# Kernel optimization log

Hardware: AMD Instinct MI355X
Metric: run time of the kernel (lower is better)

## Reference

```python
import jax, jax.numpy as jnp
import numpy as np

N_NODES = 100000
N_EDGES = 1600000
D = 128


def _gine_layer(x, src, dst, e, W1, b1, W2, b2):
    # message: relu(x_j + e_ji), aggregate: sum at destination
    m = jax.nn.relu(x[src] + e)                       # [E, D]
    agg = jax.ops.segment_sum(m, dst, num_segments=x.shape[0])  # [N, D]
    h = agg + x                                       # (1 + eps) * x_i with eps = 0
    h = jax.nn.relu(jnp.dot(h, W1) + b1)
    return jnp.dot(h, W2) + b2


def setup_inputs() -> dict:
    key = jax.random.key(0)
    ks = jax.random.split(key, 16)
    s = 0.05
    inp = {
        "x": jax.random.normal(ks[0], (N_NODES, D), dtype=jnp.float32),
        "edge_index": jax.random.randint(ks[1], (2, N_EDGES), 0, N_NODES, dtype=jnp.int64) if jax.config.jax_enable_x64 else jax.random.randint(ks[1], (2, N_EDGES), 0, N_NODES, dtype=jnp.int32),
        "edge_attr": jax.random.randint(ks[2], (N_EDGES,), 0, 100, dtype=jnp.int32),
        "edge_emb": jax.random.normal(ks[3], (100, D), dtype=jnp.float32) * s,
        "Win": jax.random.normal(ks[4], (D, D), dtype=jnp.float32) * s,
        "b_in": jnp.zeros((D,), dtype=jnp.float32),
        "W1_0": jax.random.normal(ks[5], (D, D), dtype=jnp.float32) * s,
        "b1_0": jnp.zeros((D,), dtype=jnp.float32),
        "W2_0": jax.random.normal(ks[6], (D, D), dtype=jnp.float32) * s,
        "b2_0": jnp.zeros((D,), dtype=jnp.float32),
        "W1_1": jax.random.normal(ks[7], (D, D), dtype=jnp.float32) * s,
        "b1_1": jnp.zeros((D,), dtype=jnp.float32),
        "W2_1": jax.random.normal(ks[8], (D, D), dtype=jnp.float32) * s,
        "b2_1": jnp.zeros((D,), dtype=jnp.float32),
        "Wout": jax.random.normal(ks[9], (D, 1), dtype=jnp.float32) * s,
        "b_out": jnp.zeros((1,), dtype=jnp.float32),
    }
    return inp


def reference(x, edge_index, edge_attr, edge_emb, Win, b_in,
              W1_0, b1_0, W2_0, b2_0, W1_1, b1_1, W2_1, b2_1,
              Wout, b_out):
    src, dst = edge_index[0], edge_index[1]
    e = edge_emb[edge_attr]                 # [E, D] edge-attribute embedding lookup
    h = jnp.dot(x, Win) + b_in              # input_proj
    # layer 0: GINEConv + residual add + relu (norm=none, dropout off)
    h = jax.nn.relu(_gine_layer(h, src, dst, e, W1_0, b1_0, W2_0, b2_0) + h)
    # layer 1
    h = jax.nn.relu(_gine_layer(h, src, dst, e, W1_1, b1_1, W2_1, b2_1) + h)
    # output_mlp: single Linear(hidden, 1); no final activation, no pooling
    return jnp.dot(h, Wout) + b_out
```

## Files before the change

kernel.cpp:

```cpp
#include <hip/hip_runtime.h>

#define NN 100000
#define D 128
#define CHUNK 4096
#define BCSTRIDE 392
#define AGG_BLOCKS 1024

typedef __attribute__((ext_vector_type(8))) short short8;
typedef __attribute__((ext_vector_type(8))) unsigned short ushort8;
typedef __attribute__((ext_vector_type(4))) float f32x4;

__device__ __forceinline__ float4 ld4(const float* p) { return *(const float4*)p; }

__device__ __forceinline__ unsigned short f2bf(float f) {
    unsigned int u = __float_as_uint(f);
    unsigned int r = u + 0x7fffu + ((u >> 16) & 1u);
    return (unsigned short)(r >> 16);
}
__device__ __forceinline__ float bf2f(unsigned short h) {
    return __uint_as_float(((unsigned int)h) << 16);
}
__device__ __forceinline__ int swz(int r, int c) {
    return r * 128 + ((((c >> 2) ^ (r & 7)) << 2) | (c & 3));
}

__device__ __forceinline__ void coop_gemm8(
    const unsigned int* uT,
    const unsigned short* __restrict__ Whi, const unsigned short* __restrict__ Wlo,
    int wv, int lane, int lr, int q, f32x4 acc[4])
{
    #pragma unroll
    for (int ks = 0; ks < 4; ++ks) {
        short8 ahi[4], alo[4];
        #pragma unroll
        for (int m = 0; m < 4; ++m) {
            const int row = m * 16 + lr;
            const int cb  = ks * 32 + q * 8;
            const uint4 a0 = *(const uint4*)&uT[swz(row, cb)];
            const uint4 a1 = *(const uint4*)&uT[swz(row, cb + 4)];
            const unsigned int w[8] = {a0.x, a0.y, a0.z, a0.w, a1.x, a1.y, a1.z, a1.w};
            #pragma unroll
            for (int j = 0; j < 8; ++j) {
                ahi[m][j] = (short)(w[j] >> 16);
                alo[m][j] = (short)(w[j] & 0xffffu);
            }
        }
        const int base = ((wv * 4 + ks) * 64 + lane) * 8;
        const short8 bhi = *(const short8*)&Whi[base];
        const short8 blo = *(const short8*)&Wlo[base];
        #pragma unroll
        for (int m = 0; m < 4; ++m) {
            acc[m] = __builtin_amdgcn_mfma_f32_16x16x32_bf16(alo[m], bhi, acc[m], 0, 0, 0);
            acc[m] = __builtin_amdgcn_mfma_f32_16x16x32_bf16(ahi[m], blo, acc[m], 0, 0, 0);
            acc[m] = __builtin_amdgcn_mfma_f32_16x16x32_bf16(ahi[m], bhi, acc[m], 0, 0, 0);
        }
    }
}

__device__ __forceinline__ void gemm_in_body(
    unsigned int* uT, int bid,
    const float* __restrict__ A1,
    const unsigned short* __restrict__ Whi, const unsigned short* __restrict__ Wlo,
    const float* __restrict__ bias,
    unsigned short* __restrict__ out_hi, unsigned short* __restrict__ out_lo, int N)
{
    const int t    = threadIdx.x;
    const int wv   = t >> 6;
    const int lane = t & 63;
    const int lr   = lane & 15;
    const int q    = lane >> 4;
    const int rE   = wv * 8 + (lane >> 3);
    const int cE   = (lane & 7) * 16;
    const int rowE = bid * 64 + rE;

    {
        float v[16];
        if (rowE < N) {
            const int off = rowE * D + cE;
            #pragma unroll
            for (int k = 0; k < 4; ++k) {
                const float4 x = ld4(&A1[off + k * 4]);
                v[k * 4 + 0] = x.x; v[k * 4 + 1] = x.y; v[k * 4 + 2] = x.z; v[k * 4 + 3] = x.w;
            }
        } else {
            #pragma unroll
            for (int j = 0; j < 16; ++j) v[j] = 0.f;
        }
        #pragma unroll
        for (int k = 0; k < 4; ++k) {
            unsigned int pk[4];
            #pragma unroll
            for (int j = 0; j < 4; ++j) {
                const float f = v[k * 4 + j];
                const unsigned int hi = f2bf(f);
                pk[j] = (hi << 16) | f2bf(f - bf2f((unsigned short)hi));
            }
            *(uint4*)&uT[swz(rE, cE + k * 4)] = make_uint4(pk[0], pk[1], pk[2], pk[3]);
        }
    }
    __syncthreads();

    f32x4 acc[4];
    #pragma unroll
    for (int m = 0; m < 4; ++m) acc[m] = (f32x4){0.f, 0.f, 0.f, 0.f};
    coop_gemm8(uT, Whi, Wlo, wv, lane, lr, q, acc);
    __syncthreads();

    {
        const float b = bias[wv * 16 + lr];
        #pragma unroll
        for (int m = 0; m < 4; ++m)
            #pragma unroll
            for (int r = 0; r < 4; ++r)
                uT[swz(m * 16 + q * 4 + r, wv * 16 + lr)] = __float_as_uint(acc[m][r] + b);
    }
    __syncthreads();

    if (rowE < N) {
        const int off = rowE * D + cE;
        unsigned int w[16];
        #pragma unroll
        for (int k = 0; k < 4; ++k) {
            const uint4 a = *(const uint4*)&uT[swz(rE, cE + k * 4)];
            w[k * 4 + 0] = a.x; w[k * 4 + 1] = a.y; w[k * 4 + 2] = a.z; w[k * 4 + 3] = a.w;
        }
        #pragma unroll
        for (int h8 = 0; h8 < 2; ++h8) {
            ushort8 oh, ol;
            #pragma unroll
            for (int j = 0; j < 8; ++j) {
                const float o = __uint_as_float(w[h8 * 8 + j]);
                const unsigned short h = f2bf(o);
                oh[j] = h;
                ol[j] = f2bf(o - bf2f(h));
            }
            *(ushort8*)&out_hi[off + h8 * 8] = oh;
            *(ushort8*)&out_lo[off + h8 * 8] = ol;
        }
    }
}

__global__ __launch_bounds__(256) void setup_all(
    const float* __restrict__ W0, const float* __restrict__ W1,
    const float* __restrict__ W2, const float* __restrict__ W3,
    const float* __restrict__ W4, unsigned short* __restrict__ wp,
    const float* __restrict__ emb, unsigned int* __restrict__ embp,
    int* __restrict__ binTotal)
{
    const int T = blockIdx.x * 256 + threadIdx.x;
    if (T < 5 * D * D) {
        const int w = T / (D * D);
        const int t = T % (D * D);
        const float* W = (w == 0) ? W0 : (w == 1) ? W1 : (w == 2) ? W2 : (w == 3) ? W3 : W4;
        const int j  = t & 7;
        const int L  = (t >> 3) & 63;
        const int ks = (t >> 9) & 3;
        const int nt = t >> 11;
        const float v = W[(ks * 32 + (L >> 4) * 8 + j) * D + nt * 16 + (L & 15)];
        const unsigned short h = f2bf(v);
        unsigned short* hi = wp + (size_t)w * 2 * D * D;
        hi[t] = h;
        hi[D * D + t] = f2bf(v - bf2f(h));
    } else if (T < 5 * D * D + 6400) {
        const int i = T - 5 * D * D;
        embp[i] = (unsigned int)f2bf(emb[i * 2]) | ((unsigned int)f2bf(emb[i * 2 + 1]) << 16);
    } else if (T < 5 * D * D + 6400 + BCSTRIDE) {
        binTotal[T - 5 * D * D - 6400] = 0;
    }
}

__global__ __launch_bounds__(512, 8) void fuse_count_gemm(
    const int* __restrict__ dst, int* __restrict__ blkcnt,
    int* __restrict__ binTotal, int E, int nbins, int csrB,
    const float* __restrict__ A1,
    const unsigned short* __restrict__ Whi, const unsigned short* __restrict__ Wlo,
    const float* __restrict__ bias,
    unsigned short* __restrict__ out_hi, unsigned short* __restrict__ out_lo,
    int N, int gemmBase)
{
    __shared__ __align__(16) unsigned int uT[64 * 128];
    if ((int)blockIdx.x < csrB) {
        int* hist = (int*)uT;
        const int t = threadIdx.x;
        const int i = blockIdx.x;
        for (int k = t; k < nbins; k += 512) hist[k] = 0;
        __syncthreads();
        const int e0 = i * CHUNK;
        const int e1 = min(E, e0 + CHUNK);
        for (int e = e0 + t; e < e1; e += 512) atomicAdd(&hist[dst[e] >> 8], 1);
        __syncthreads();
        for (int k = t; k < nbins; k += 512) {
            const int c = hist[k];
            blkcnt[i * BCSTRIDE + k] = c;
            if (c) atomicAdd(&binTotal[k], c);
        }
    } else {
        gemm_in_body(uT, blockIdx.x - csrB + gemmBase, A1, Whi, Wlo, bias, out_hi, out_lo, N);
    }
}

__global__ __launch_bounds__(512) void bin_scan(
    const int* __restrict__ binTotal, int* __restrict__ binStart,
    int* __restrict__ binCursor, int nbins)
{
    __shared__ int s[512];
    const int t = threadIdx.x;
    const int v = (t < nbins) ? binTotal[t] : 0;
    s[t] = v;
    __syncthreads();
    for (int off = 1; off < 512; off <<= 1) {
        const int x = (t >= off) ? s[t - off] : 0;
        __syncthreads();
        s[t] += x;
        __syncthreads();
    }
    if (t < nbins) { binStart[t] = s[t] - v; binCursor[t] = s[t] - v; }
    if (t == 0)    binStart[nbins] = s[511];
}

__global__ __launch_bounds__(512, 8) void fuse_scatter_gemm(
    const int* __restrict__ src, const int* __restrict__ dst,
    const int* __restrict__ attr, const int* __restrict__ blkcnt,
    int* __restrict__ binCursor, int2* __restrict__ binned, int E, int nbins, int csrB,
    const float* __restrict__ A1,
    const unsigned short* __restrict__ Whi, const unsigned short* __restrict__ Wlo,
    const float* __restrict__ bias,
    unsigned short* __restrict__ out_hi, unsigned short* __restrict__ out_lo,
    int N, int gemmBase)
{
    __shared__ __align__(16) unsigned int uT[64 * 128];
    if ((int)blockIdx.x < csrB) {
        int* cur = (int*)uT;
        const int t = threadIdx.x;
        const int i = blockIdx.x;
        for (int k = t; k < nbins; k += 512) {
            const int c = blkcnt[i * BCSTRIDE + k];
            if (c) cur[k] = atomicAdd(&binCursor[k], c);
        }
        __syncthreads();
        const int e0 = i * CHUNK;
        const int e1 = min(E, e0 + CHUNK);
        for (int e = e0 + t; e < e1; e += 512) {
            const int d = dst[e];
            const int p = atomicAdd(&cur[d >> 8], 1);
            binned[p] = make_int2(src[e] | (attr[e] << 20), d);
        }
    } else {
        gemm_in_body(uT, blockIdx.x - csrB + gemmBase, A1, Whi, Wlo, bias, out_hi, out_lo, N);
    }
}

__global__ __launch_bounds__(512, 8) void fuse_build_gemm(
    const int2* __restrict__ binned, const int* __restrict__ binStart,
    int* __restrict__ rowptr, int* __restrict__ epack, int csrB,
    const float* __restrict__ A1,
    const unsigned short* __restrict__ Whi, const unsigned short* __restrict__ Wlo,
    const float* __restrict__ bias,
    unsigned short* __restrict__ out_hi, unsigned short* __restrict__ out_lo,
    int N, int gemmBase)
{
    __shared__ __align__(16) unsigned int uT[64 * 128];
    if ((int)blockIdx.x < csrB) {
        int* hist = (int*)uT;
        int* scn  = (int*)uT + 256;
        int* curn = (int*)uT + 512;
        const int t = threadIdx.x;
        const int b = blockIdx.x;
        if (t < 256) hist[t] = 0;
        __syncthreads();
        const int ebeg = binStart[b];
        const int eend = binStart[b + 1];
        for (int e = ebeg + t; e < eend; e += 512) atomicAdd(&hist[binned[e].y & 255], 1);
        __syncthreads();
        if (t < 256) scn[t] = hist[t];
        __syncthreads();
        for (int off = 1; off < 256; off <<= 1) {
            int x = 0;
            if (t < 256 && t >= off) x = scn[t - off];
            __syncthreads();
            if (t < 256) scn[t] += x;
            __syncthreads();
        }
        if (t < 256) {
            const int node = b * 256 + t;
            if (node < N) rowptr[node] = ebeg + scn[t];
            curn[t] = ebeg + scn[t] - hist[t];
        }
        __syncthreads();
        for (int e = ebeg + t; e < eend; e += 512) {
            const int2 v = binned[e];
            const int p = atomicAdd(&curn[v.y & 255], 1);
            epack[p] = v.x;
        }
    } else {
        gemm_in_body(uT, blockIdx.x - csrB + gemmBase, A1, Whi, Wlo, bias, out_hi, out_lo, N);
    }
}

template<bool LAST>
__global__ __launch_bounds__(512, 8) void mlp_fused(
    const float* __restrict__ agg,
    const unsigned short* h_hi, const unsigned short* h_lo,
    const unsigned short* __restrict__ W1hi, const unsigned short* __restrict__ W1lo,
    const float* __restrict__ b1,
    const unsigned short* __restrict__ W2hi, const unsigned short* __restrict__ W2lo,
    const float* __restrict__ b2,
    unsigned short* out_hi, unsigned short* out_lo,
    const float* __restrict__ Wout, const float* __restrict__ bout,
    float* __restrict__ outv, int N)
{
    __shared__ __align__(16) unsigned int uT[64 * 128];
    const int t    = threadIdx.x;
    const int wv   = t >> 6;
    const int lane = t & 63;
    const int lr   = lane & 15;
    const int q    = lane >> 4;
    const int rE   = wv * 8 + (lane >> 3);
    const int cE   = (lane & 7) * 16;
    const int rowE = blockIdx.x * 64 + rE;

    {
        float v[16];
        if (rowE < N) {
            const int off = rowE * D + cE;
            #pragma unroll
            for (int k = 0; k < 4; ++k) {
                const float4 x = ld4(&agg[off + k * 4]);
                v[k * 4 + 0] = x.x; v[k * 4 + 1] = x.y; v[k * 4 + 2] = x.z; v[k * 4 + 3] = x.w;
            }
            #pragma unroll
            for (int h8 = 0; h8 < 2; ++h8) {
                const ushort8 hh = *(const ushort8*)&h_hi[off + h8 * 8];
                const ushort8 ll = *(const ushort8*)&h_lo[off + h8 * 8];
                #pragma unroll
                for (int j = 0; j < 8; ++j) v[h8 * 8 + j] += bf2f(hh[j]) + bf2f(ll[j]);
            }
        } else {
            #pragma unroll
            for (int j = 0; j < 16; ++j) v[j] = 0.f;
        }
        #pragma unroll
        for (int k = 0; k < 4; ++k) {
            unsigned int pk[4];
            #pragma unroll
            for (int j = 0; j < 4; ++j) {
                const float f = v[k * 4 + j];
                const unsigned int hi = f2bf(f);
                pk[j] = (hi << 16) | f2bf(f - bf2f((unsigned short)hi));
            }
            *(uint4*)&uT[swz(rE, cE + k * 4)] = make_uint4(pk[0], pk[1], pk[2], pk[3]);
        }
    }
    __syncthreads();

    f32x4 acc[4];
    #pragma unroll
    for (int m = 0; m < 4; ++m) acc[m] = (f32x4){0.f, 0.f, 0.f, 0.f};
    coop_gemm8(uT, W1hi, W1lo, wv, lane, lr, q, acc);
    __syncthreads();

    {
        const float b = b1[wv * 16 + lr];
        #pragma unroll
        for (int m = 0; m < 4; ++m)
            #pragma unroll
            for (int r = 0; r < 4; ++r) {
                const float o = fmaxf(acc[m][r] + b, 0.f);
                const unsigned int hi = f2bf(o);
                const unsigned int lo = f2bf(o - bf2f((unsigned short)hi));
                uT[swz(m * 16 + q * 4 + r, wv * 16 + lr)] = (hi << 16) | lo;
            }
    }
    __syncthreads();

    f32x4 acc2[4];
    #pragma unroll
    for (int m = 0; m < 4; ++m) acc2[m] = (f32x4){0.f, 0.f, 0.f, 0.f};
    coop_gemm8(uT, W2hi, W2lo, wv, lane, lr, q, acc2);
    __syncthreads();

    {
        const float b = b2[wv * 16 + lr];
        #pragma unroll
        for (int m = 0; m < 4; ++m)
            #pragma unroll
            for (int r = 0; r < 4; ++r)
                uT[swz(m * 16 + q * 4 + r, wv * 16 + lr)] = __float_as_uint(acc2[m][r] + b);
    }
    __syncthreads();

    if (LAST) {
        float accv = 0.f;
        if (rowE < N) {
            const int off = rowE * D + cE;
            unsigned int w[16];
            #pragma unroll
            for (int k = 0; k < 4; ++k) {
                const uint4 a = *(const uint4*)&uT[swz(rE, cE + k * 4)];
                w[k * 4 + 0] = a.x; w[k * 4 + 1] = a.y; w[k * 4 + 2] = a.z; w[k * 4 + 3] = a.w;
            }
            #pragma unroll
            for (int h8 = 0; h8 < 2; ++h8) {
                const ushort8 hh = *(const ushort8*)&h_hi[off + h8 * 8];
                const ushort8 ll = *(const ushort8*)&h_lo[off + h8 * 8];
                const float4 w0 = ld4(&Wout[cE + h8 * 8]);
                const float4 w1 = ld4(&Wout[cE + h8 * 8 + 4]);
                float o[8];
                #pragma unroll
                for (int j = 0; j < 8; ++j)
                    o[j] = fmaxf(__uint_as_float(w[h8 * 8 + j]) + bf2f(hh[j]) + bf2f(ll[j]), 0.f);
                accv += o[0] * w0.x + o[1] * w0.y + o[2] * w0.z + o[3] * w0.w;
                accv += o[4] * w1.x + o[5] * w1.y + o[6] * w1.z + o[7] * w1.w;
            }
        }
        accv += __shfl_xor(accv, 1);
        accv += __shfl_xor(accv, 2);
        accv += __shfl_xor(accv, 4);
        if ((lane & 7) == 0 && rowE < N) outv[rowE] = accv + bout[0];
    } else if (rowE < N) {
        const int off = rowE * D + cE;
        unsigned int w[16];
        #pragma unroll
        for (int k = 0; k < 4; ++k) {
            const uint4 a = *(const uint4*)&uT[swz(rE, cE + k * 4)];
            w[k * 4 + 0] = a.x; w[k * 4 + 1] = a.y; w[k * 4 + 2] = a.z; w[k * 4 + 3] = a.w;
        }
        #pragma unroll
        for (int h8 = 0; h8 < 2; ++h8) {
            const ushort8 hh = *(const ushort8*)&h_hi[off + h8 * 8];
            const ushort8 ll = *(const ushort8*)&h_lo[off + h8 * 8];
            ushort8 oh, ol;
            #pragma unroll
            for (int j = 0; j < 8; ++j) {
                const float o = fmaxf(__uint_as_float(w[h8 * 8 + j]) + bf2f(hh[j]) + bf2f(ll[j]), 0.f);
                const unsigned short h = f2bf(o);
                oh[j] = h;
                ol[j] = f2bf(o - bf2f(h));
            }
            *(ushort8*)&out_hi[off + h8 * 8] = oh;
            *(ushort8*)&out_lo[off + h8 * 8] = ol;
        }
    }
}

__global__ __launch_bounds__(512) void aggregate(
    const unsigned int* __restrict__ hu,
    const int* __restrict__ rowptr, const int* __restrict__ epack,
    const unsigned int* __restrict__ embp, float* __restrict__ agg, int N)
{
    __shared__ unsigned int semb[100 * 64];
    const int t = threadIdx.x;
    for (int i = t; i < 100 * 64; i += 512) semb[i] = embp[i];
    __syncthreads();

    const int wv   = t >> 6;
    const int lane = t & 63;

    for (int node = blockIdx.x * 8 + wv; node < N; node += AGG_BLOCKS * 8) {
        int start = (node == 0) ? 0 : rowptr[node - 1];
        int end   = rowptr[node];
        start = __builtin_amdgcn_readfirstlane(start);
        end   = __builtin_amdgcn_readfirstlane(end);

        float ax = 0.f, ay = 0.f;
        int j = start;

        for (; j < end && (j & 3); ++j) {
            const int p0 = __builtin_amdgcn_readfirstlane(epack[j]);
            const unsigned int u0 = hu[(p0 & 0xFFFFF) * 64 + lane];
            const unsigned int v0 = semb[(p0 >> 20) * 64 + lane];
            ax += fmaxf(__uint_as_float(u0 << 16) + __uint_as_float(v0 << 16), 0.f);
            ay += fmaxf(__uint_as_float(u0 & 0xffff0000u) + __uint_as_float(v0 & 0xffff0000u), 0.f);
        }

        for (; j + 7 < end; j += 8) {
            const int4 pk0 = *(const int4*)&epack[j];
            const int4 pk1 = *(const int4*)&epack[j + 4];
            int p[8];
            p[0] = __builtin_amdgcn_readfirstlane(pk0.x);
            p[1] = __builtin_amdgcn_readfirstlane(pk0.y);
            p[2] = __builtin_amdgcn_readfirstlane(pk0.z);
            p[3] = __builtin_amdgcn_readfirstlane(pk0.w);
            p[4] = __builtin_amdgcn_readfirstlane(pk1.x);
            p[5] = __builtin_amdgcn_readfirstlane(pk1.y);
            p[6] = __builtin_amdgcn_readfirstlane(pk1.z);
            p[7] = __builtin_amdgcn_readfirstlane(pk1.w);
            unsigned int u[8], v[8];
            #pragma unroll
            for (int k = 0; k < 8; ++k) u[k] = hu[(p[k] & 0xFFFFF) * 64 + lane];
            #pragma unroll
            for (int k = 0; k < 8; ++k) v[k] = semb[(p[k] >> 20) * 64 + lane];
            #pragma unroll
            for (int k = 0; k < 8; ++k) {
                ax += fmaxf(__uint_as_float(u[k] << 16) + __uint_as_float(v[k] << 16), 0.f);
                ay += fmaxf(__uint_as_float(u[k] & 0xffff0000u) + __uint_as_float(v[k] & 0xffff0000u), 0.f);
            }
        }

        if (j + 3 < end) {
            const int4 pk0 = *(const int4*)&epack[j];
            int p[4];
            p[0] = __builtin_amdgcn_readfirstlane(pk0.x);
            p[1] = __builtin_amdgcn_readfirstlane(pk0.y);
            p[2] = __builtin_amdgcn_readfirstlane(pk0.z);
            p[3] = __builtin_amdgcn_readfirstlane(pk0.w);
            unsigned int u[4], v[4];
            #pragma unroll
            for (int k = 0; k < 4; ++k) u[k] = hu[(p[k] & 0xFFFFF) * 64 + lane];
            #pragma unroll
            for (int k = 0; k < 4; ++k) v[k] = semb[(p[k] >> 20) * 64 + lane];
            #pragma unroll
            for (int k = 0; k < 4; ++k) {
                ax += fmaxf(__uint_as_float(u[k] << 16) + __uint_as_float(v[k] << 16), 0.f);
                ay += fmaxf(__uint_as_float(u[k] & 0xffff0000u) + __uint_as_float(v[k] & 0xffff0000u), 0.f);
            }
            j += 4;
        }

        for (; j < end; ++j) {
            const int p0 = __builtin_amdgcn_readfirstlane(epack[j]);
            const unsigned int u0 = hu[(p0 & 0xFFFFF) * 64 + lane];
            const unsigned int v0 = semb[(p0 >> 20) * 64 + lane];
            ax += fmaxf(__uint_as_float(u0 << 16) + __uint_as_float(v0 << 16), 0.f);
            ay += fmaxf(__uint_as_float(u0 & 0xffff0000u) + __uint_as_float(v0 & 0xffff0000u), 0.f);
        }

        float2 o; o.x = ax; o.y = ay;
        ((float2*)agg)[node * 64 + lane] = o;
    }
}

extern "C" void kernel_launch(void* const* d_in, const int* in_sizes, int n_in,
                              void* d_out, int out_size, void* d_ws, size_t ws_size,
                              hipStream_t stream)
{
    const float* x     = (const float*)d_in[0];
    const int*   ei    = (const int*)  d_in[1];
    const int*   attr  = (const int*)  d_in[2];
    const float* emb   = (const float*)d_in[3];
    const float* Win   = (const float*)d_in[4];
    const float* b_in  = (const float*)d_in[5];
    const float* W1_0  = (const float*)d_in[6];
    const float* b1_0  = (const float*)d_in[7];
    const float* W2_0  = (const float*)d_in[8];
    const float* b2_0  = (const float*)d_in[9];
    const float* W1_1  = (const float*)d_in[10];
    const float* b1_1  = (const float*)d_in[11];
    const float* W2_1  = (const float*)d_in[12];
    const float* b2_1  = (const float*)d_in[13];
    const float* Wout  = (const float*)d_in[14];
    const float* b_out = (const float*)d_in[15];
    float* out = (float*)d_out;

    const int N = NN;
    const int E = in_sizes[2];
    const int* srcp = ei;
    const int* dstp = ei + E;
    const int nbins = (N + 255) >> 8;
    const int eblocks = (E + CHUNK - 1) / CHUNK;

    unsigned short* h_hi = (unsigned short*)d_ws;
    unsigned short* h_lo = h_hi + (size_t)N * D;
    float* agg    = (float*)(h_lo + (size_t)N * D);
    int*   rowptr = (int*)(agg + (size_t)N * D);
    int*   epack  = rowptr + N;
    unsigned short* wp = (unsigned short*)(epack + E);
    unsigned short* Whi[5], *Wlo[5];
    for (int i = 0; i < 5; ++i) {
        Whi[i] = wp + (size_t)i * 2 * D * D;
        Wlo[i] = Whi[i] + D * D;
    }
    unsigned int* embp = (unsigned int*)(wp + 5 * 2 * D * D);
    int2* binned    = (int2*)agg;
    int*  blkcnt    = (int*)(binned + E);
    int*  binTotal  = blkcnt + eblocks * BCSTRIDE;
    int*  binStart  = binTotal + BCSTRIDE;
    int*  binCursor = binStart + BCSTRIDE;

    const int fgrid = (N + 63) / 64;
    const int sgrid = (5 * D * D + 6400 + BCSTRIDE + 255) / 256;

    const int G1 = 200;
    const int G2 = 700;
    const int G3 = fgrid - G1 - G2;

    setup_all<<<sgrid, dim3(256), 0, stream>>>(Win, W1_0, W2_0, W1_1, W2_1, wp, emb, embp, binTotal);

    fuse_count_gemm<<<eblocks + G1, dim3(512), 0, stream>>>(
        dstp, blkcnt, binTotal, E, nbins, eblocks,
        x, Whi[0], Wlo[0], b_in, h_hi, h_lo, N, 0);
    bin_scan<<<1, 512, 0, stream>>>(binTotal, binStart, binCursor, nbins);
    fuse_scatter_gemm<<<eblocks + G2, dim3(512), 0, stream>>>(
        srcp, dstp, attr, blkcnt, binCursor, binned, E, nbins, eblocks,
        x, Whi[0], Wlo[0], b_in, h_hi, h_lo, N, G1);
    fuse_build_gemm<<<nbins + G3, dim3(512), 0, stream>>>(
        binned, binStart, rowptr, epack, nbins,
        x, Whi[0], Wlo[0], b_in, h_hi, h_lo, N, G1 + G2);

    aggregate<<<AGG_BLOCKS, dim3(512), 0, stream>>>(
        (const unsigned int*)h_hi, rowptr, epack, embp, agg, N);
    mlp_fused<false><<<fgrid, dim3(512), 0, stream>>>(
        agg, h_hi, h_lo, Whi[1], Wlo[1], b1_0, Whi[2], Wlo[2], b2_0,
        h_hi, h_lo, nullptr, nullptr, nullptr, N);

    aggregate<<<AGG_BLOCKS, dim3(512), 0, stream>>>(
        (const unsigned int*)h_hi, rowptr, epack, embp, agg, N);
    mlp_fused<true><<<fgrid, dim3(512), 0, stream>>>(
        agg, h_hi, h_lo, Whi[3], Wlo[3], b1_1, Whi[4], Wlo[4], b2_1,
        nullptr, nullptr, Wout, b_out, out, N);
}
```

Measured before the change: 418.9 us.

## Split wavefront into two half-waves each gathering a different edge with 8-byte loads

The aggregate kernel now gives each half of a 64-lane wavefront a different edge. Each lane loads a uint2 (four bf16 features) per edge instead of one uint32, so two edges are gathered per load instruction. The two half-wave partial sums are combined with a cross-half shuffle and written as float4. The goal is more memory-level parallelism and fewer load instructions per edge in the gather-bound aggregation, at the cost of a shuffle reduction and idle half-waves on odd edge tails. The renames in the GEMM helper are cosmetic.

```diff
diff --git a/kernel.cpp b/kernel.cpp
--- a/kernel.cpp
+++ b/kernel.cpp
@@ -20,6 +20,9 @@
 __device__ __forceinline__ float bf2f(unsigned short h) {
     return __uint_as_float(((unsigned int)h) << 16);
 }
+__device__ __forceinline__ float blo(unsigned int u) { return __uint_as_float(u << 16); }
+__device__ __forceinline__ float bhi(unsigned int u) { return __uint_as_float(u & 0xffff0000u); }
+
 __device__ __forceinline__ int swz(int r, int c) {
     return r * 128 + ((((c >> 2) ^ (r & 7)) << 2) | (c & 3));
 }
@@ -46,13 +49,13 @@
             }
         }
         const int base = ((wv * 4 + ks) * 64 + lane) * 8;
-        const short8 bhi = *(const short8*)&Whi[base];
-        const short8 blo = *(const short8*)&Wlo[base];
+        const short8 bhi8 = *(const short8*)&Whi[base];
+        const short8 blo8 = *(const short8*)&Wlo[base];
         #pragma unroll
         for (int m = 0; m < 4; ++m) {
-            acc[m] = __builtin_amdgcn_mfma_f32_16x16x32_bf16(alo[m], bhi, acc[m], 0, 0, 0);
-            acc[m] = __builtin_amdgcn_mfma_f32_16x16x32_bf16(ahi[m], blo, acc[m], 0, 0, 0);
-            acc[m] = __builtin_amdgcn_mfma_f32_16x16x32_bf16(ahi[m], bhi, acc[m], 0, 0, 0);
+            acc[m] = __builtin_amdgcn_mfma_f32_16x16x32_bf16(alo[m], bhi8, acc[m], 0, 0, 0);
+            acc[m] = __builtin_amdgcn_mfma_f32_16x16x32_bf16(ahi[m], blo8, acc[m], 0, 0, 0);
+            acc[m] = __builtin_amdgcn_mfma_f32_16x16x32_bf16(ahi[m], bhi8, acc[m], 0, 0, 0);
         }
     }
 }
@@ -455,6 +458,11 @@
 
     const int wv   = t >> 6;
     const int lane = t & 63;
+    const int half = lane >> 5;
+    const int k    = lane & 31;
+
+    const uint2* hu2   = (const uint2*)hu;
+    const uint2* semb2 = (const uint2*)semb;
 
     for (int node = blockIdx.x * 8 + wv; node < N; node += AGG_BLOCKS * 8) {
         int start = (node == 0) ? 0 : rowptr[node - 1];
@@ -462,71 +470,74 @@
         start = __builtin_amdgcn_readfirstlane(start);
         end   = __builtin_amdgcn_readfirstlane(end);
 
-        float ax = 0.f, ay = 0.f;
+        float a0 = 0.f, a1 = 0.f, a2 = 0.f, a3 = 0.f;
         int j = start;
 
         for (; j < end && (j & 3); ++j) {
-            const int p0 = __builtin_amdgcn_readfirstlane(epack[j]);
-            const unsigned int u0 = hu[(p0 & 0xFFFFF) * 64 + lane];
-            const unsigned int v0 = semb[(p0 >> 20) * 64 + lane];
-            ax += fmaxf(__uint_as_float(u0 << 16) + __uint_as_float(v0 << 16), 0.f);
-            ay += fmaxf(__uint_as_float(u0 & 0xffff0000u) + __uint_as_float(v0 & 0xffff0000u), 0.f);
-        }
-
-        for (; j + 7 < end; j += 8) {
-            const int4 pk0 = *(const int4*)&epack[j];
-            const int4 pk1 = *(const int4*)&epack[j + 4];
-            int p[8];
-            p[0] = __builtin_amdgcn_readfirstlane(pk0.x);
-            p[1] = __builtin_amdgcn_readfirstlane(pk0.y);
-            p[2] = __builtin_amdgcn_readfirstlane(pk0.z);
-            p[3] = __builtin_amdgcn_readfirstlane(pk0.w);
-            p[4] = __builtin_amdgcn_readfirstlane(pk1.x);
-            p[5] = __builtin_amdgcn_readfirstlane(pk1.y);
-            p[6] = __builtin_amdgcn_readfirstlane(pk1.z);
-            p[7] = __builtin_amdgcn_readfirstlane(pk1.w);
-            unsigned int u[8], v[8];
-            #pragma unroll
-            for (int k = 0; k < 8; ++k) u[k] = hu[(p[k] & 0xFFFFF) * 64 + lane];
-            #pragma unroll
-            for (int k = 0; k < 8; ++k) v[k] = semb[(p[k] >> 20) * 64 + lane];
-            #pragma unroll
-            for (int k = 0; k < 8; ++k) {
-                ax += fmaxf(__uint_as_float(u[k] << 16) + __uint_as_float(v[k] << 16), 0.f);
-                ay += fmaxf(__uint_as_float(u[k] & 0xffff0000u) + __uint_as_float(v[k] & 0xffff0000u), 0.f);
-            }
-        }
-
-        if (j + 3 < end) {
-            const int4 pk0 = *(const int4*)&epack[j];
-            int p[4];
-            p[0] = __builtin_amdgcn_readfirstlane(pk0.x);
-            p[1] = __builtin_amdgcn_readfirstlane(pk0.y);
-            p[2] = __builtin_amdgcn_readfirstlane(pk0.z);
-            p[3] = __builtin_amdgcn_readfirstlane(pk0.w);
-            unsigned int u[4], v[4];
-            #pragma unroll
-            for (int k = 0; k < 4; ++k) u[k] = hu[(p[k] & 0xFFFFF) * 64 + lane];
-            #pragma unroll
-            for (int k = 0; k < 4; ++k) v[k] = semb[(p[k] >> 20) * 64 + lane];
-            #pragma unroll
-            for (int k = 0; k < 4; ++k) {
-                ax += fmaxf(__uint_as_float(u[k] << 16) + __uint_as_float(v[k] << 16), 0.f);
-                ay += fmaxf(__uint_as_float(u[k] & 0xffff0000u) + __uint_as_float(v[k] & 0xffff0000u), 0.f);
-            }
-            j += 4;
-        }
-
-        for (; j < end; ++j) {
-            const int p0 = __builtin_amdgcn_readfirstlane(epack[j]);
-            const unsigned int u0 = hu[(p0 & 0xFFFFF) * 64 + lane];
-            const unsigned int v0 = semb[(p0 >> 20) * 64 + lane];
-            ax += fmaxf(__uint_as_float(u0 << 16) + __uint_as_float(v0 << 16), 0.f);
-            ay += fmaxf(__uint_as_float(u0 & 0xffff0000u) + __uint_as_float(v0 & 0xffff0000u), 0.f);
-        }
-
-        float2 o; o.x = ax; o.y = ay;
-        ((float2*)agg)[node * 64 + lane] = o;
+            const int p = __builtin_amdgcn_readfirstlane(epack[j]);
+            if (!half) {
+                const uint2 u = hu2[(p & 0xFFFFF) * 32 + k];
+                const uint2 v = semb2[(p >> 20) * 32 + k];
+                a0 += fmaxf(blo(u.x) + blo(v.x), 0.f);
+                a1 += fmaxf(bhi(u.x) + bhi(v.x), 0.f);
+                a2 += fmaxf(blo(u.y) + blo(v.y), 0.f);
+                a3 += fmaxf(bhi(u.y) + bhi(v.y), 0.f);
+            }
+        }
+
+        for (; j + 3 < end; j += 4) {
+            const int4 pk = *(const int4*)&epack[j];
+            const int pA0 = __builtin_amdgcn_readfirstlane(pk.x);
+            const int pB0 = __builtin_amdgcn_readfirstlane(pk.y);
+            const int pA1 = __builtin_amdgcn_readfirstlane(pk.z);
+            const int pB1 = __builtin_amdgcn_readfirstlane(pk.w);
+            const int p0 = half ? pB0 : pA0;
+            const int p1 = half ? pB1 : pA1;
+            const uint2 u0 = hu2[(p0 & 0xFFFFF) * 32 + k];
+            const uint2 u1 = hu2[(p1 & 0xFFFFF) * 32 + k];
+            const uint2 v0 = semb2[(p0 >> 20) * 32 + k];
+            const uint2 v1 = semb2[(p1 >> 20) * 32 + k];
+            a0 += fmaxf(blo(u0.x) + blo(v0.x), 0.f);
+            a1 += fmaxf(bhi(u0.x) + bhi(v0.x), 0.f);
+            a2 += fmaxf(blo(u0.y) + blo(v0.y), 0.f);
+            a3 += fmaxf(bhi(u0.y) + bhi(v0.y), 0.f);
+            a0 += fmaxf(blo(u1.x) + blo(v1.x), 0.f);
+            a1 += fmaxf(bhi(u1.x) + bhi(v1.x), 0.f);
+            a2 += fmaxf(blo(u1.y) + blo(v1.y), 0.f);
+            a3 += fmaxf(bhi(u1.y) + bhi(v1.y), 0.f);
+        }
+
+        if (j + 1 < end) {
+            const int2 pk = *(const int2*)&epack[j];
+            const int pA = __builtin_amdgcn_readfirstlane(pk.x);
+            const int pB = __builtin_amdgcn_readfirstlane(pk.y);
+            const int p = half ? pB : pA;
+            const uint2 u = hu2[(p & 0xFFFFF) * 32 + k];
+            const uint2 v = semb2[(p >> 20) * 32 + k];
+            a0 += fmaxf(blo(u.x) + blo(v.x), 0.f);
+            a1 += fmaxf(bhi(u.x) + bhi(v.x), 0.f);
+            a2 += fmaxf(blo(u.y) + blo(v.y), 0.f);
+            a3 += fmaxf(bhi(u.y) + bhi(v.y), 0.f);
+            j += 2;
+        }
+        if (j < end) {
+            const int p = __builtin_amdgcn_readfirstlane(epack[j]);
+            if (!half) {
+                const uint2 u = hu2[(p & 0xFFFFF) * 32 + k];
+                const uint2 v = semb2[(p >> 20) * 32 + k];
+                a0 += fmaxf(blo(u.x) + blo(v.x), 0.f);
+                a1 += fmaxf(bhi(u.x) + bhi(v.x), 0.f);
+                a2 += fmaxf(blo(u.y) + blo(v.y), 0.f);
+                a3 += fmaxf(bhi(u.y) + bhi(v.y), 0.f);
+            }
+        }
+
+        a0 += __shfl_xor(a0, 32);
+        a1 += __shfl_xor(a1, 32);
+        a2 += __shfl_xor(a2, 32);
+        a3 += __shfl_xor(a3, 32);
+        if (!half)
+            *(float4*)&agg[node * D + k * 4] = make_float4(a0, a1, a2, a3);
     }
 }
 
```

New measurement: 420.8 us. No clear change (+0.5%).

## Fuse neighbor aggregation into per-layer MLP kernel with ping-pong node buffers

Applied to the files above, without the earlier changes.

Merges the separate aggregate kernel into the MLP kernel: each block gathers messages for its 64 destination nodes (8 per wave) and writes the sums straight into shared memory before the two GEMMs. This removes the fp32 agg round trip through global memory and one launch per layer. Because other blocks still read the layer input, the layer-0 output now goes to a second hi/lo buffer carved from the old agg space instead of being written in place. Edge embeddings are now read from global/cache rather than staged in LDS, and load balancing moves from a grid-stride loop to a fixed 64-node block, which may suffer from degree imbalance.

```diff
diff --git a/kernel.cpp b/kernel.cpp
--- a/kernel.cpp
+++ b/kernel.cpp
@@ -4,7 +4,6 @@
 #define D 128
 #define CHUNK 4096
 #define BCSTRIDE 392
-#define AGG_BLOCKS 1024
 
 typedef __attribute__((ext_vector_type(8))) short short8;
 typedef __attribute__((ext_vector_type(8))) unsigned short ushort8;
@@ -20,6 +19,9 @@
 __device__ __forceinline__ float bf2f(unsigned short h) {
     return __uint_as_float(((unsigned int)h) << 16);
 }
+__device__ __forceinline__ float blo(unsigned int u) { return __uint_as_float(u << 16); }
+__device__ __forceinline__ float bhi(unsigned int u) { return __uint_as_float(u & 0xffff0000u); }
+
 __device__ __forceinline__ int swz(int r, int c) {
     return r * 128 + ((((c >> 2) ^ (r & 7)) << 2) | (c & 3));
 }
@@ -46,13 +48,13 @@
             }
         }
         const int base = ((wv * 4 + ks) * 64 + lane) * 8;
-        const short8 bhi = *(const short8*)&Whi[base];
-        const short8 blo = *(const short8*)&Wlo[base];
+        const short8 bhi8 = *(const short8*)&Whi[base];
+        const short8 blo8 = *(const short8*)&Wlo[base];
         #pragma unroll
         for (int m = 0; m < 4; ++m) {
-            acc[m] = __builtin_amdgcn_mfma_f32_16x16x32_bf16(alo[m], bhi, acc[m], 0, 0, 0);
-            acc[m] = __builtin_amdgcn_mfma_f32_16x16x32_bf16(ahi[m], blo, acc[m], 0, 0, 0);
-            acc[m] = __builtin_amdgcn_mfma_f32_16x16x32_bf16(ahi[m], bhi, acc[m], 0, 0, 0);
+            acc[m] = __builtin_amdgcn_mfma_f32_16x16x32_bf16(alo[m], bhi8, acc[m], 0, 0, 0);
+            acc[m] = __builtin_amdgcn_mfma_f32_16x16x32_bf16(ahi[m], blo8, acc[m], 0, 0, 0);
+            acc[m] = __builtin_amdgcn_mfma_f32_16x16x32_bf16(ahi[m], bhi8, acc[m], 0, 0, 0);
         }
     }
 }
@@ -298,14 +300,15 @@
 }
 
 template<bool LAST>
-__global__ __launch_bounds__(512, 8) void mlp_fused(
-    const float* __restrict__ agg,
-    const unsigned short* h_hi, const unsigned short* h_lo,
+__global__ __launch_bounds__(512, 8) void gine_fused(
+    const unsigned short* __restrict__ h_hi, const unsigned short* __restrict__ h_lo,
+    const int* __restrict__ rowptr, const int* __restrict__ epack,
+    const unsigned int* __restrict__ embp,
     const unsigned short* __restrict__ W1hi, const unsigned short* __restrict__ W1lo,
     const float* __restrict__ b1,
     const unsigned short* __restrict__ W2hi, const unsigned short* __restrict__ W2lo,
     const float* __restrict__ b2,
-    unsigned short* out_hi, unsigned short* out_lo,
+    unsigned short* __restrict__ out_hi, unsigned short* __restrict__ out_lo,
     const float* __restrict__ Wout, const float* __restrict__ bout,
     float* __restrict__ outv, int N)
 {
@@ -319,144 +322,12 @@
     const int cE   = (lane & 7) * 16;
     const int rowE = blockIdx.x * 64 + rE;
 
-    {
-        float v[16];
-        if (rowE < N) {
-            const int off = rowE * D + cE;
-            #pragma unroll
-            for (int k = 0; k < 4; ++k) {
-                const float4 x = ld4(&agg[off + k * 4]);
-                v[k * 4 + 0] = x.x; v[k * 4 + 1] = x.y; v[k * 4 + 2] = x.z; v[k * 4 + 3] = x.w;
-            }
-            #pragma unroll
-            for (int h8 = 0; h8 < 2; ++h8) {
-                const ushort8 hh = *(const ushort8*)&h_hi[off + h8 * 8];
-                const ushort8 ll = *(const ushort8*)&h_lo[off + h8 * 8];
-                #pragma unroll
-                for (int j = 0; j < 8; ++j) v[h8 * 8 + j] += bf2f(hh[j]) + bf2f(ll[j]);
-            }
-        } else {
-            #pragma unroll
-            for (int j = 0; j < 16; ++j) v[j] = 0.f;
-        }
-        #pragma unroll
-        for (int k = 0; k < 4; ++k) {
-            unsigned int pk[4];
-            #pragma unroll
-            for (int j = 0; j < 4; ++j) {
-                const float f = v[k * 4 + j];
-                const unsigned int hi = f2bf(f);
-                pk[j] = (hi << 16) | f2bf(f - bf2f((unsigned short)hi));
-            }
-            *(uint4*)&uT[swz(rE, cE + k * 4)] = make_uint4(pk[0], pk[1], pk[2], pk[3]);
-        }
-    }
-    __syncthreads();
-
-    f32x4 acc[4];
-    #pragma unroll
-    for (int m = 0; m < 4; ++m) acc[m] = (f32x4){0.f, 0.f, 0.f, 0.f};
-    coop_gemm8(uT, W1hi, W1lo, wv, lane, lr, q, acc);
-    __syncthreads();
-
-    {
-        const float b = b1[wv * 16 + lr];
-        #pragma unroll
-        for (int m = 0; m < 4; ++m)
-            #pragma unroll
-            for (int r = 0; r < 4; ++r) {
-                const float o = fmaxf(acc[m][r] + b, 0.f);
-                const unsigned int hi = f2bf(o);
-                const unsigned int lo = f2bf(o - bf2f((unsigned short)hi));
-                uT[swz(m * 16 + q * 4 + r, wv * 16 + lr)] = (hi << 16) | lo;
-            }
-    }
-    __syncthreads();
-
-    f32x4 acc2[4];
-    #pragma unroll
-    for (int m = 0; m < 4; ++m) acc2[m] = (f32x4){0.f, 0.f, 0.f, 0.f};
-    coop_gemm8(uT, W2hi, W2lo, wv, lane, lr, q, acc2);
-    __syncthreads();
-
-    {
-        const float b = b2[wv * 16 + lr];
-        #pragma unroll
-        for (int m = 0; m < 4; ++m)
-            #pragma unroll
-            for (int r = 0; r < 4; ++r)
-                uT[swz(m * 16 + q * 4 + r, wv * 16 + lr)] = __float_as_uint(acc2[m][r] + b);
-    }
-    __syncthreads();
-
-    if (LAST) {
-        float accv = 0.f;
-        if (rowE < N) {
-            const int off = rowE * D + cE;
-            unsigned int w[16];
-            #pragma unroll
-            for (int k = 0; k < 4; ++k) {
-                const uint4 a = *(const uint4*)&uT[swz(rE, cE + k * 4)];
-                w[k * 4 + 0] = a.x; w[k * 4 + 1] = a.y; w[k * 4 + 2] = a.z; w[k * 4 + 3] = a.w;
-            }
-            #pragma unroll
-            for (int h8 = 0; h8 < 2; ++h8) {
-                const ushort8 hh = *(const ushort8*)&h_hi[off + h8 * 8];
-                const ushort8 ll = *(const ushort8*)&h_lo[off + h8 * 8];
-                const float4 w0 = ld4(&Wout[cE + h8 * 8]);
-                const float4 w1 = ld4(&Wout[cE + h8 * 8 + 4]);
-                float o[8];
-                #pragma unroll
-                for (int j = 0; j < 8; ++j)
-                    o[j] = fmaxf(__uint_as_float(w[h8 * 8 + j]) + bf2f(hh[j]) + bf2f(ll[j]), 0.f);
-                accv += o[0] * w0.x + o[1] * w0.y + o[2] * w0.z + o[3] * w0.w;
-                accv += o[4] * w1.x + o[5] * w1.y + o[6] * w1.z + o[7] * w1.w;
-            }
-        }
-        accv += __shfl_xor(accv, 1);
-        accv += __shfl_xor(accv, 2);
-        accv += __shfl_xor(accv, 4);
-        if ((lane & 7) == 0 && rowE < N) outv[rowE] = accv + bout[0];
-    } else if (rowE < N) {
-        const int off = rowE * D + cE;
-        unsigned int w[16];
-        #pragma unroll
-        for (int k = 0; k < 4; ++k) {
-            const uint4 a = *(const uint4*)&uT[swz(rE, cE + k * 4)];
-            w[k * 4 + 0] = a.x; w[k * 4 + 1] = a.y; w[k * 4 + 2] = a.z; w[k * 4 + 3] = a.w;
-        }
-        #pragma unroll
-        for (int h8 = 0; h8 < 2; ++h8) {
-            const ushort8 hh = *(const ushort8*)&h_hi[off + h8 * 8];
-            const ushort8 ll = *(const ushort8*)&h_lo[off + h8 * 8];
-            ushort8 oh, ol;
-            #pragma unroll
-            for (int j = 0; j < 8; ++j) {
-                const float o = fmaxf(__uint_as_float(w[h8 * 8 + j]) + bf2f(hh[j]) + bf2f(ll[j]), 0.f);
-                const unsigned short h = f2bf(o);
-                oh[j] = h;
-                ol[j] = f2bf(o - bf2f(h));
-            }
-            *(ushort8*)&out_hi[off + h8 * 8] = oh;
-            *(ushort8*)&out_lo[off + h8 * 8] = ol;
-        }
-    }
-}
-
-__global__ __launch_bounds__(512) void aggregate(
-    const unsigned int* __restrict__ hu,
-    const int* __restrict__ rowptr, const int* __restrict__ epack,
-    const unsigned int* __restrict__ embp, float* __restrict__ agg, int N)
-{
-    __shared__ unsigned int semb[100 * 64];
-    const int t = threadIdx.x;
-    for (int i = t; i < 100 * 64; i += 512) semb[i] = embp[i];
-    __syncthreads();
-
-    const int wv   = t >> 6;
-    const int lane = t & 63;
-
-    for (int node = blockIdx.x * 8 + wv; node < N; node += AGG_BLOCKS * 8) {
+    const unsigned int* hu = (const unsigned int*)h_hi;
+
+    for (int i = 0; i < 8; ++i) {
+        const int row  = wv * 8 + i;
+        const int node = blockIdx.x * 64 + row;
+        if (node >= N) break;
         int start = (node == 0) ? 0 : rowptr[node - 1];
         int end   = rowptr[node];
         start = __builtin_amdgcn_readfirstlane(start);
@@ -468,9 +339,9 @@
         for (; j < end && (j & 3); ++j) {
             const int p0 = __builtin_amdgcn_readfirstlane(epack[j]);
             const unsigned int u0 = hu[(p0 & 0xFFFFF) * 64 + lane];
-            const unsigned int v0 = semb[(p0 >> 20) * 64 + lane];
-            ax += fmaxf(__uint_as_float(u0 << 16) + __uint_as_float(v0 << 16), 0.f);
-            ay += fmaxf(__uint_as_float(u0 & 0xffff0000u) + __uint_as_float(v0 & 0xffff0000u), 0.f);
+            const unsigned int v0 = embp[(p0 >> 20) * 64 + lane];
+            ax += fmaxf(blo(u0) + blo(v0), 0.f);
+            ay += fmaxf(bhi(u0) + bhi(v0), 0.f);
         }
 
         for (; j + 7 < end; j += 8) {
@@ -489,11 +360,11 @@
             #pragma unroll
             for (int k = 0; k < 8; ++k) u[k] = hu[(p[k] & 0xFFFFF) * 64 + lane];
             #pragma unroll
-            for (int k = 0; k < 8; ++k) v[k] = semb[(p[k] >> 20) * 64 + lane];
+            for (int k = 0; k < 8; ++k) v[k] = embp[(p[k] >> 20) * 64 + lane];
             #pragma unroll
             for (int k = 0; k < 8; ++k) {
-                ax += fmaxf(__uint_as_float(u[k] << 16) + __uint_as_float(v[k] << 16), 0.f);
-                ay += fmaxf(__uint_as_float(u[k] & 0xffff0000u) + __uint_as_float(v[k] & 0xffff0000u), 0.f);
+                ax += fmaxf(blo(u[k]) + blo(v[k]), 0.f);
+                ay += fmaxf(bhi(u[k]) + bhi(v[k]), 0.f);
             }
         }
 
@@ -508,11 +379,11 @@
             #pragma unroll
             for (int k = 0; k < 4; ++k) u[k] = hu[(p[k] & 0xFFFFF) * 64 + lane];
             #pragma unroll
-            for (int k = 0; k < 4; ++k) v[k] = semb[(p[k] >> 20) * 64 + lane];
+            for (int k = 0; k < 4; ++k) v[k] = embp[(p[k] >> 20) * 64 + lane];
             #pragma unroll
             for (int k = 0; k < 4; ++k) {
-                ax += fmaxf(__uint_as_float(u[k] << 16) + __uint_as_float(v[k] << 16), 0.f);
-                ay += fmaxf(__uint_as_float(u[k] & 0xffff0000u) + __uint_as_float(v[k] & 0xffff0000u), 0.f);
+                ax += fmaxf(blo(u[k]) + blo(v[k]), 0.f);
+                ay += fmaxf(bhi(u[k]) + bhi(v[k]), 0.f);
             }
             j += 4;
         }
@@ -520,13 +391,138 @@
         for (; j < end; ++j) {
             const int p0 = __builtin_amdgcn_readfirstlane(epack[j]);
             const unsigned int u0 = hu[(p0 & 0xFFFFF) * 64 + lane];
-            const unsigned int v0 = semb[(p0 >> 20) * 64 + lane];
-            ax += fmaxf(__uint_as_float(u0 << 16) + __uint_as_float(v0 << 16), 0.f);
-            ay += fmaxf(__uint_as_float(u0 & 0xffff0000u) + __uint_as_float(v0 & 0xffff0000u), 0.f);
-        }
-
-        float2 o; o.x = ax; o.y = ay;
-        ((float2*)agg)[node * 64 + lane] = o;
+            const unsigned int v0 = embp[(p0 >> 20) * 64 + lane];
+            ax += fmaxf(blo(u0) + blo(v0), 0.f);
+            ay += fmaxf(bhi(u0) + bhi(v0), 0.f);
+        }
+
+        *(float2*)&uT[swz(row, 2 * lane)] = make_float2(ax, ay);
+    }
+
+    {
+        float v[16];
+        if (rowE < N) {
+            #pragma unroll
+            for (int k = 0; k < 4; ++k) {
+                const uint4 a = *(const uint4*)&uT[swz(rE, cE + k * 4)];
+                v[k * 4 + 0] = __uint_as_float(a.x);
+                v[k * 4 + 1] = __uint_as_float(a.y);
+                v[k * 4 + 2] = __uint_as_float(a.z);
+                v[k * 4 + 3] = __uint_as_float(a.w);
+            }
+            const int off = rowE * D + cE;
+            #pragma unroll
+            for (int h8 = 0; h8 < 2; ++h8) {
+                const ushort8 hh = *(const ushort8*)&h_hi[off + h8 * 8];
+                const ushort8 ll = *(const ushort8*)&h_lo[off + h8 * 8];
+                #pragma unroll
+                for (int j = 0; j < 8; ++j) v[h8 * 8 + j] += bf2f(hh[j]) + bf2f(ll[j]);
+            }
+        } else {
+            #pragma unroll
+            for (int j = 0; j < 16; ++j) v[j] = 0.f;
+        }
+        #pragma unroll
+        for (int k = 0; k < 4; ++k) {
+            unsigned int pk[4];
+            #pragma unroll
+            for (int j = 0; j < 4; ++j) {
+                const float f = v[k * 4 + j];
+                const unsigned int hi = f2bf(f);
+                pk[j] = (hi << 16) | f2bf(f - bf2f((unsigned short)hi));
+            }
+            *(uint4*)&uT[swz(rE, cE + k * 4)] = make_uint4(pk[0], pk[1], pk[2], pk[3]);
+        }
+    }
+    __syncthreads();
+
+    f32x4 acc[4];
+    #pragma unroll
+    for (int m = 0; m < 4; ++m) acc[m] = (f32x4){0.f, 0.f, 0.f, 0.f};
+    coop_gemm8(uT, W1hi, W1lo, wv, lane, lr, q, acc);
+    __syncthreads();
+
+    {
+        const float b = b1[wv * 16 + lr];
+        #pragma unroll
+        for (int m = 0; m < 4; ++m)
+            #pragma unroll
+            for (int r = 0; r < 4; ++r) {
+                const float o = fmaxf(acc[m][r] + b, 0.f);
+                const unsigned int hi = f2bf(o);
+                const unsigned int lo = f2bf(o - bf2f((unsigned short)hi));
+                uT[swz(m * 16 + q * 4 + r, wv * 16 + lr)] = (hi << 16) | lo;
+            }
+    }
+    __syncthreads();
+
+    f32x4 acc2[4];
+    #pragma unroll
+    for (int m = 0; m < 4; ++m) acc2[m] = (f32x4){0.f, 0.f, 0.f, 0.f};
+    coop_gemm8(uT, W2hi, W2lo, wv, lane, lr, q, acc2);
+    __syncthreads();
+
+    {
+        const float b = b2[wv * 16 + lr];
+        #pragma unroll
+        for (int m = 0; m < 4; ++m)
+            #pragma unroll
+            for (int r = 0; r < 4; ++r)
+                uT[swz(m * 16 + q * 4 + r, wv * 16 + lr)] = __float_as_uint(acc2[m][r] + b);
+    }
+    __syncthreads();
+
+    if (LAST) {
+        float accv = 0.f;
+        if (rowE < N) {
+            const int off = rowE * D + cE;
+            unsigned int w[16];
+            #pragma unroll
+            for (int k = 0; k < 4; ++k) {
+                const uint4 a = *(const uint4*)&uT[swz(rE, cE + k * 4)];
+                w[k * 4 + 0] = a.x; w[k * 4 + 1] = a.y; w[k * 4 + 2] = a.z; w[k * 4 + 3] = a.w;
+            }
+            #pragma unroll
+            for (int h8 = 0; h8 < 2; ++h8) {
+                const ushort8 hh = *(const ushort8*)&h_hi[off + h8 * 8];
+                const ushort8 ll = *(const ushort8*)&h_lo[off + h8 * 8];
+                const float4 w0 = ld4(&Wout[cE + h8 * 8]);
+                const float4 w1 = ld4(&Wout[cE + h8 * 8 + 4]);
+                float o[8];
+                #pragma unroll
+                for (int j = 0; j < 8; ++j)
+                    o[j] = fmaxf(__uint_as_float(w[h8 * 8 + j]) + bf2f(hh[j]) + bf2f(ll[j]), 0.f);
+                accv += o[0] * w0.x + o[1] * w0.y + o[2] * w0.z + o[3] * w0.w;
+                accv += o[4] * w1.x + o[5] * w1.y + o[6] * w1.z + o[7] * w1.w;
+            }
+        }
+        accv += __shfl_xor(accv, 1);
+        accv += __shfl_xor(accv, 2);
+        accv += __shfl_xor(accv, 4);
+        if ((lane & 7) == 0 && rowE < N) outv[rowE] = accv + bout[0];
+    } else if (rowE < N) {
+        const int off = rowE * D + cE;
+        unsigned int w[16];
+        #pragma unroll
+        for (int k = 0; k < 4; ++k) {
+            const uint4 a = *(const uint4*)&uT[swz(rE, cE + k * 4)];
+            w[k * 4 + 0] = a.x; w[k * 4 + 1] = a.y; w[k * 4 + 2] = a.z; w[k * 4 + 3] = a.w;
+        }
+        #pragma unroll
+        for (int h8 = 0; h8 < 2; ++h8) {
+            const ushort8 hh = *(const ushort8*)&h_hi[off + h8 * 8];
+            const ushort8 ll = *(const ushort8*)&h_lo[off + h8 * 8];
+            ushort8 oh, ol;
+            #pragma unroll
+            for (int j = 0; j < 8; ++j) {
+                const float o = fmaxf(__uint_as_float(w[h8 * 8 + j]) + bf2f(hh[j]) + bf2f(ll[j]), 0.f);
+                const unsigned short h = f2bf(o);
+                oh[j] = h;
+                ol[j] = f2bf(o - bf2f(h));
+            }
+            *(ushort8*)&out_hi[off + h8 * 8] = oh;
+            *(ushort8*)&out_lo[off + h8 * 8] = ol;
+        }
     }
 }
 
@@ -561,8 +557,8 @@
 
     unsigned short* h_hi = (unsigned short*)d_ws;
     unsigned short* h_lo = h_hi + (size_t)N * D;
-    float* agg    = (float*)(h_lo + (size_t)N * D);
-    int*   rowptr = (int*)(agg + (size_t)N * D);
+    float* aggspace = (float*)(h_lo + (size_t)N * D);
+    int*   rowptr = (int*)(aggspace + (size_t)N * D);
     int*   epack  = rowptr + N;
     unsigned short* wp = (unsigned short*)(epack + E);
     unsigned short* Whi[5], *Wlo[5];
@@ -571,11 +567,13 @@
         Wlo[i] = Whi[i] + D * D;
     }
     unsigned int* embp = (unsigned int*)(wp + 5 * 2 * D * D);
-    int2* binned    = (int2*)agg;
+    int2* binned    = (int2*)aggspace;
     int*  blkcnt    = (int*)(binned + E);
     int*  binTotal  = blkcnt + eblocks * BCSTRIDE;
     int*  binStart  = binTotal + BCSTRIDE;
     int*  binCursor = binStart + BCSTRIDE;
+    unsigned short* hB_hi = (unsigned short*)aggspace;
+    unsigned short* hB_lo = hB_hi + (size_t)N * D;
 
     const int fgrid = (N + 63) / 64;
     const int sgrid = (5 * D * D + 6400 + BCSTRIDE + 255) / 256;
@@ -597,15 +595,13 @@
         binned, binStart, rowptr, epack, nbins,
         x, Whi[0], Wlo[0], b_in, h_hi, h_lo, N, G1 + G2);
 
-    aggregate<<<AGG_BLOCKS, dim3(512), 0, stream>>>(
-        (const unsigned int*)h_hi, rowptr, epack, embp, agg, N);
-    mlp_fused<false><<<fgrid, dim3(512), 0, stream>>>(
-        agg, h_hi, h_lo, Whi[1], Wlo[1], b1_0, Whi[2], Wlo[2], b2_0,
-        h_hi, h_lo, nullptr, nullptr, nullptr, N);
-
-    aggregate<<<AGG_BLOCKS, dim3(512), 0, stream>>>(
-        (const unsigned int*)h_hi, rowptr, epack, embp, agg, N);
-    mlp_fused<true><<<fgrid, dim3(512), 0, stream>>>(
-        agg, h_hi, h_lo, Whi[3], Wlo[3], b1_1, Whi[4], Wlo[4], b2_1,
+    gine_fused<false><<<fgrid, dim3(512), 0, stream>>>(
+        h_hi, h_lo, rowptr, epack, embp,
+        Whi[1], Wlo[1], b1_0, Whi[2], Wlo[2], b2_0,
+        hB_hi, hB_lo, nullptr, nullptr, nullptr, N);
+
+    gine_fused<true><<<fgrid, dim3(512), 0, stream>>>(
+        hB_hi, hB_lo, rowptr, epack, embp,
+        Whi[3], Wlo[3], b1_1, Whi[4], Wlo[4], b2_1,
         nullptr, nullptr, Wout, b_out, out, N);
 }
```

Result: faster. 397.3 us (-5.1%).
